# Optimization experiments

Hardware: AMD Instinct MI355X
Metric: run time of the kernel (lower is better)

## Reference

```python
import jax, jax.numpy as jnp
import numpy as np

N = 400000          # num nodes == num edges (required by the module's final cat)
E = 400000
NODE_DIM = 64
BOND_DIM = 16
HIDDEN = 128
DEPTH = 5


def _sanitize(t):
    return jnp.nan_to_num(t, nan=0.0, posinf=1000.0, neginf=-1000.0)


def setup_inputs() -> dict:
    key = jax.random.key(0)
    ks = jax.random.split(key, 10)
    x = jax.random.normal(ks[0], (N, NODE_DIM), dtype=jnp.float32)
    edge_attr = jax.random.normal(ks[1], (E, BOND_DIM), dtype=jnp.float32)
    edge_index = jax.random.randint(ks[2], (2, E), 0, N, dtype=jnp.int32)
    # edges come in reverse pairs (2k, 2k+1): force endpoints consistent
    src = edge_index[0]
    dst = edge_index[1]
    # make edge 2k+1 the reverse of edge 2k
    src = src.reshape(E // 2, 2)
    dst = dst.reshape(E // 2, 2)
    src = jnp.stack([src[:, 0], dst[:, 0]], axis=1).reshape(E)
    dst = jnp.stack([dst[:, 0], src.reshape(E // 2, 2)[:, 0]], axis=1).reshape(E)
    edge_index = jnp.stack([src, dst], axis=0)
    rev_edge_index = jnp.arange(E, dtype=jnp.int32) ^ 1
    # parameters (kaiming-normal-ish scale, zero bias as in reset_parameters)
    def kaiming(k, fan_in, fan_out):
        std = np.sqrt(2.0 / fan_out)  # mode='fan_out'
        return std * jax.random.normal(k, (fan_in, fan_out), dtype=jnp.float32)
    W_i = kaiming(ks[3], NODE_DIM + BOND_DIM, HIDDEN)
    b_i = jnp.zeros((HIDDEN,), dtype=jnp.float32)
    W_h = kaiming(ks[4], HIDDEN, HIDDEN)
    b_h = jnp.zeros((HIDDEN,), dtype=jnp.float32)
    W_o = kaiming(ks[5], NODE_DIM + HIDDEN, HIDDEN)
    b_o = jnp.zeros((HIDDEN,), dtype=jnp.float32)
    return {"x": x, "edge_index": edge_index, "edge_attr": edge_attr,
            "rev_edge_index": rev_edge_index,
            "W_i": W_i, "b_i": b_i, "W_h": W_h, "b_h": b_h,
            "W_o": W_o, "b_o": b_o}


def reference(x, edge_index, edge_attr, rev_edge_index, W_i, b_i, W_h, b_h, W_o, b_o):
    src, dst = edge_index[0], edge_index[1]
    # h0: per-edge hidden state [E, H]
    h0 = jax.nn.relu(jnp.concatenate([x[src], edge_attr], axis=1) @ W_i + b_i)
    h = h0
    for _ in range(1, DEPTH):
        # scatter-add incoming messages at dst node ids (rows >= N stay 0)
        m = jnp.zeros_like(h).at[dst].add(h)
        # subtract reverse-edge message at src node ids (all rev indices valid)
        m = m.at[src].add(-h[rev_edge_index])
        m = _sanitize(m) @ W_h + b_h
        h = jax.nn.relu(h0 + m)   # dropout is identity in eval / p handled as 0
    m_final = jnp.zeros_like(h).at[dst].add(h)
    h_cat = jnp.concatenate([x, _sanitize(m_final)], axis=1)  # requires N == E
    out = jax.nn.relu(h_cat @ W_o + b_o)
    return _sanitize(out)
```

## Files before the change

### kernel.cpp

```cpp
#include <hip/hip_runtime.h>


typedef __bf16 bf16x8 __attribute__((ext_vector_type(8)));
typedef float f32x4 __attribute__((ext_vector_type(4)));
typedef unsigned short u16;
typedef unsigned int u32;

#define LDW  104
#define LDW2 200
#define LDT  136
#define SLOTS 16

static __device__ __forceinline__ u16 f32_to_bf16(float f) {
    union { float f; u32 u; } c; c.f = f;
    u32 u = c.u;
    u += 0x7FFFu + ((u >> 16) & 1u);
    return (u16)(u >> 16);
}
static __device__ __forceinline__ u32 pk2(float a, float b) {
    return (u32)f32_to_bf16(a) | (((u32)f32_to_bf16(b)) << 16);
}
static __device__ __forceinline__ uint4 pack8(float4 a, float4 b) {
    return make_uint4(pk2(a.x, a.y), pk2(a.z, a.w), pk2(b.x, b.y), pk2(b.z, b.w));
}


__global__ __launch_bounds__(256) void k_prep(
    const float4* __restrict__ x4, const float4* __restrict__ ea4,
    const float* __restrict__ Wi, const float* __restrict__ Wo,
    uint4* __restrict__ cnt16, uint4* __restrict__ xb4,
    uint4* __restrict__ eab4, u16* __restrict__ WiT, u16* __restrict__ WoT,
    int nCnt16, int nX8, int nEa8)
{
    const int gtid = blockIdx.x * 256 + threadIdx.x;
    const int stride = gridDim.x * 256;
    const uint4 z = make_uint4(0, 0, 0, 0);
    for (int i = gtid; i < nCnt16; i += stride) cnt16[i] = z;
    for (int i = gtid; i < nX8; i += stride)
        xb4[i] = pack8(x4[2 * i], x4[2 * i + 1]);
    for (int i = gtid; i < nEa8; i += stride)
        eab4[i] = pack8(ea4[2 * i], ea4[2 * i + 1]);
    for (int i = gtid; i < 128 * LDW; i += stride) {
        int n = i / LDW, k = i - n * LDW;
        WiT[i] = (k < 80) ? f32_to_bf16(Wi[k * 128 + n]) : (u16)0;
    }
    for (int i = gtid; i < 128 * LDW2; i += stride) {
        int n = i / LDW2, k = i - n * LDW2;
        WoT[i] = (k < 192) ? f32_to_bf16(Wo[k * 128 + n]) : (u16)0;
    }
}

__global__ __launch_bounds__(256) void k_fill(
    const int* __restrict__ ei, int* __restrict__ counts,
    int2* __restrict__ slot, int E)
{
    const int e = blockIdx.x * 256 + threadIdx.x;
    if (e < E) {
        const int dst = ei[E + e];
        const int pos = atomicAdd(&counts[dst], 1);
        if (pos < SLOTS)
            slot[(size_t)dst * SLOTS + pos] = make_int2(ei[e], e);
    }
}

__global__ __launch_bounds__(512) void k_main(
    const u16* __restrict__ xb, const u16* __restrict__ eab,
    const int2* __restrict__ slot, const int* __restrict__ deg,
    const uint4* __restrict__ WiT16, const uint4* __restrict__ WoT16,
    const float* __restrict__ bi, const float* __restrict__ bh,
    const float* __restrict__ bo, float* __restrict__ out, int Nn)
{
    __shared__ __align__(16) u16 sWi[128 * LDW];
    __shared__ __align__(16) u16 sWo[128 * LDW2];
    __shared__ __align__(16) u16 sTr[8][16 * LDT];

    const int tid  = threadIdx.x;
    const int wave = tid >> 6;
    const int lane = tid & 63;
    const int col  = lane & 15;
    const int quad = lane >> 4;

    #pragma unroll 2
    for (int i = tid; i < 128 * LDW / 8; i += 512)
        ((uint4*)sWi)[i] = WiT16[i];
    #pragma unroll 2
    for (int i = tid; i < 128 * LDW2 / 8; i += 512)
        ((uint4*)sWo)[i] = WoT16[i];
    __syncthreads();

    float bias_i[8], bias_h[8], bias_o[8];
    #pragma unroll
    for (int nt = 0; nt < 8; ++nt) {
        bias_i[nt] = bi[nt * 16 + col];
        bias_h[nt] = bh[nt * 16 + col];
        bias_o[nt] = bo[nt * 16 + col];
    }

    u16* tr = &sTr[wave][0];
    const uint4 z4 = make_uint4(0, 0, 0, 0);

    for (int t4 = 0; t4 < 4; ++t4) {
        const int row0 = blockIdx.x * 512 + wave * 64 + t4 * 16;
        const int nA   = row0 + col;
        int degA = (nA < Nn) ? min(deg[nA], SLOTS) : 0;
        int degC[4];
        #pragma unroll
        for (int rg = 0; rg < 4; ++rg) {
            int n = row0 + quad * 4 + rg;
            degC[rg] = (n < Nn) ? min(deg[n], SLOTS) : 0;
        }
        int tmax = degA;
        tmax = max(tmax, __shfl_xor(tmax, 1));
        tmax = max(tmax, __shfl_xor(tmax, 2));
        tmax = max(tmax, __shfl_xor(tmax, 4));
        tmax = max(tmax, __shfl_xor(tmax, 8));

        f32x4 m[8];
        #pragma unroll
        for (int nt = 0; nt < 8; ++nt) m[nt] = (f32x4)0.0f;

        for (int t = 0; t < tmax; ++t) {
            uint4 Af0 = z4, Af1 = z4, Af2 = z4;
            if (t < degA) {
                const int2 se = slot[(size_t)nA * SLOTS + t];
                const u16* xr = xb + (size_t)se.x * 64;
                Af0 = *(const uint4*)(xr + quad * 8);
                Af1 = *(const uint4*)(xr + 32 + quad * 8);
                if (quad < 2)
                    Af2 = *(const uint4*)(eab + (size_t)se.y * 16 + quad * 8);
            }
            f32x4 acc[8];
            #pragma unroll
            for (int nt = 0; nt < 8; ++nt) acc[nt] = (f32x4)0.0f;
            const uint4 Af[3] = {Af0, Af1, Af2};
            #pragma unroll
            for (int ks = 0; ks < 3; ++ks) {
                bf16x8 a = __builtin_bit_cast(bf16x8, Af[ks]);
                #pragma unroll
                for (int nt = 0; nt < 8; ++nt) {
                    bf16x8 b = __builtin_bit_cast(bf16x8,
                        *(const uint4*)(&sWi[(nt * 16 + col) * LDW + ks * 32 + quad * 8]));
                    acc[nt] = __builtin_amdgcn_mfma_f32_16x16x32_bf16(a, b, acc[nt], 0, 0, 0);
                }
            }
            #pragma unroll
            for (int nt = 0; nt < 8; ++nt) {
                #pragma unroll
                for (int rg = 0; rg < 4; ++rg) {
                    float h = fmaxf(fmaxf(acc[nt][rg] + bias_i[nt], 0.0f)
                                    + bias_h[nt], 0.0f);
                    m[nt][rg] += (t < degC[rg]) ? h : 0.0f;
                }
            }
        }

        asm volatile("s_waitcnt lgkmcnt(0)" ::: "memory");
        #pragma unroll
        for (int nt = 0; nt < 8; ++nt) {
            #pragma unroll
            for (int rg = 0; rg < 4; ++rg)
                tr[(quad * 4 + rg) * LDT + nt * 16 + col] = f32_to_bf16(m[nt][rg]);
        }
        asm volatile("s_waitcnt lgkmcnt(0)" ::: "memory");
        __builtin_amdgcn_sched_barrier(0);

        const u16* xrs = xb + (size_t)min(nA, Nn - 1) * 64;
        uint4 Bf[6];
        Bf[0] = *(const uint4*)(xrs + quad * 8);
        Bf[1] = *(const uint4*)(xrs + 32 + quad * 8);
        #pragma unroll
        for (int ks = 2; ks < 6; ++ks)
            Bf[ks] = *(const uint4*)(&tr[col * LDT + (ks - 2) * 32 + quad * 8]);

        f32x4 acc2[8];
        #pragma unroll
        for (int nt = 0; nt < 8; ++nt) acc2[nt] = (f32x4)0.0f;
        #pragma unroll
        for (int ks = 0; ks < 6; ++ks) {
            bf16x8 a = __builtin_bit_cast(bf16x8, Bf[ks]);
            #pragma unroll
            for (int nt = 0; nt < 8; ++nt) {
                bf16x8 b = __builtin_bit_cast(bf16x8,
                    *(const uint4*)(&sWo[(nt * 16 + col) * LDW2 + ks * 32 + quad * 8]));
                acc2[nt] = __builtin_amdgcn_mfma_f32_16x16x32_bf16(a, b, acc2[nt], 0, 0, 0);
            }
        }

        #pragma unroll
        for (int rg = 0; rg < 4; ++rg) {
            int node = row0 + quad * 4 + rg;
            if (node < Nn) {
                float* orow = out + (size_t)node * 128;
                #pragma unroll
                for (int nt = 0; nt < 8; ++nt) {
                    float o = fmaxf(acc2[nt][rg] + bias_o[nt], 0.0f);
                    float op = __shfl_xor(o, 1);
                    if ((col & 1) == 0)
                        *(float2*)(orow + nt * 16 + col) = make_float2(o, op);
                }
            }
        }
    }
}


__global__ __launch_bounds__(256) void k_zero_fb(uint4* __restrict__ out, int n16)
{
    const uint4 z = make_uint4(0, 0, 0, 0);
    for (int i = blockIdx.x * blockDim.x + threadIdx.x; i < n16;
         i += gridDim.x * blockDim.x)
        out[i] = z;
}

__global__ __launch_bounds__(256) void k_edge_fb(
    const float* __restrict__ x, const float* __restrict__ ea,
    const int* __restrict__ ei, const float* __restrict__ Wi,
    const float* __restrict__ bi, const float* __restrict__ bh,
    float* __restrict__ macc, int E)
{
    __shared__ __align__(16) u16 sW[128 * LDW];
    const int tid  = threadIdx.x;
    const int wave = tid >> 6;
    const int lane = tid & 63;
    const int col  = lane & 15;
    const int quad = lane >> 4;

    for (int i = tid; i < 96 * 128; i += 256) {
        int k = i >> 7, n = i & 127;
        sW[n * LDW + k] = (k < 80) ? f32_to_bf16(Wi[i]) : (u16)0;
    }
    __syncthreads();

    float bias_i[8], bias_h[8];
    #pragma unroll
    for (int nt = 0; nt < 8; ++nt) {
        bias_i[nt] = bi[nt * 16 + col];
        bias_h[nt] = bh[nt * 16 + col];
    }

    for (int t = 0; t < 4; ++t) {
        const int e0 = blockIdx.x * 256 + wave * 64 + t * 16;
        const int eidx = e0 + col;
        const int ec = (eidx < E) ? eidx : (E - 1);
        const int src = ei[ec];
        const float* xr = x + (size_t)src * 64;
        uint4 A0 = pack8(*(const float4*)(xr + quad * 8),
                         *(const float4*)(xr + quad * 8 + 4));
        uint4 A1 = pack8(*(const float4*)(xr + 32 + quad * 8),
                         *(const float4*)(xr + 32 + quad * 8 + 4));
        uint4 A2 = make_uint4(0, 0, 0, 0);
        if (quad < 2) {
            const float* er = ea + (size_t)ec * 16 + quad * 8;
            A2 = pack8(*(const float4*)er, *(const float4*)(er + 4));
        }

        f32x4 acc[8];
        #pragma unroll
        for (int nt = 0; nt < 8; ++nt) acc[nt] = (f32x4)0.0f;
        const uint4 Af[3] = {A0, A1, A2};
        #pragma unroll
        for (int ks = 0; ks < 3; ++ks) {
            bf16x8 a = __builtin_bit_cast(bf16x8, Af[ks]);
            #pragma unroll
            for (int nt = 0; nt < 8; ++nt) {
                bf16x8 b = __builtin_bit_cast(bf16x8,
                    *(const uint4*)(&sW[(nt * 16 + col) * LDW + ks * 32 + quad * 8]));
                acc[nt] = __builtin_amdgcn_mfma_f32_16x16x32_bf16(a, b, acc[nt], 0, 0, 0);
            }
        }
        #pragma unroll
        for (int rg = 0; rg < 4; ++rg) {
            int e = e0 + quad * 4 + rg;
            if (e < E) {
                int dst = ei[E + e];
                float* mrow = macc + (size_t)dst * 128;
                #pragma unroll
                for (int nt = 0; nt < 8; ++nt) {
                    float h = fmaxf(fmaxf(acc[nt][rg] + bias_i[nt], 0.0f)
                                    + bias_h[nt], 0.0f);
                    atomicAdd(mrow + nt * 16 + col, h);
                }
            }
        }
    }
}

__global__ __launch_bounds__(256) void k_node_fb(
    const float* __restrict__ x, const float* __restrict__ Wo,
    const float* __restrict__ bo, float* __restrict__ outv, int Nn)
{
    __shared__ __align__(16) u16 sW[128 * LDW2];
    const int tid  = threadIdx.x;
    const int wave = tid >> 6;
    const int lane = tid & 63;
    const int col  = lane & 15;
    const int quad = lane >> 4;

    for (int i = tid; i < 192 * 128; i += 256) {
        int k = i >> 7, n = i & 127;
        sW[n * LDW2 + k] = f32_to_bf16(Wo[i]);
    }
    __syncthreads();

    float bias[8];
    #pragma unroll
    for (int nt = 0; nt < 8; ++nt) bias[nt] = bo[nt * 16 + col];

    for (int t = 0; t < 4; ++t) {
        const int row0 = blockIdx.x * 256 + wave * 64 + t * 16;
        const int nodea = row0 + col;
        const int na = (nodea < Nn) ? nodea : (Nn - 1);
        const float* xr = x + (size_t)na * 64;
        uint4 Af[6];
        Af[0] = pack8(*(const float4*)(xr + quad * 8),
                      *(const float4*)(xr + quad * 8 + 4));
        Af[1] = pack8(*(const float4*)(xr + 32 + quad * 8),
                      *(const float4*)(xr + 32 + quad * 8 + 4));
        const float* mr = outv + (size_t)na * 128;
        #pragma unroll
        for (int ks = 2; ks < 6; ++ks) {
            const float* p = mr + (ks - 2) * 32 + quad * 8;
            Af[ks] = pack8(*(const float4*)p, *(const float4*)(p + 4));
        }

        f32x4 acc[8];
        #pragma unroll
        for (int nt = 0; nt < 8; ++nt) acc[nt] = (f32x4)0.0f;
        #pragma unroll
        for (int ks = 0; ks < 6; ++ks) {
            bf16x8 a = __builtin_bit_cast(bf16x8, Af[ks]);
            #pragma unroll
            for (int nt = 0; nt < 8; ++nt) {
                bf16x8 b = __builtin_bit_cast(bf16x8,
                    *(const uint4*)(&sW[(nt * 16 + col) * LDW2 + ks * 32 + quad * 8]));
                acc[nt] = __builtin_amdgcn_mfma_f32_16x16x32_bf16(a, b, acc[nt], 0, 0, 0);
            }
        }
        #pragma unroll
        for (int rg = 0; rg < 4; ++rg) {
            int node = row0 + quad * 4 + rg;
            if (node < Nn) {
                float* orow = outv + (size_t)node * 128;
                #pragma unroll
                for (int nt = 0; nt < 8; ++nt)
                    orow[nt * 16 + col] = fmaxf(acc[nt][rg] + bias[nt], 0.0f);
            }
        }
    }
}


extern "C" void kernel_launch(void* const* d_in, const int* in_sizes, int n_in,
                              void* d_out, int out_size, void* d_ws, size_t ws_size,
                              hipStream_t stream)
{
    const float* x  = (const float*)d_in[0];
    const int*   ei = (const int*)d_in[1];
    const float* ea = (const float*)d_in[2];
    const float* Wi = (const float*)d_in[4];
    const float* bi = (const float*)d_in[5];
    const float* bh = (const float*)d_in[7];
    const float* Wo = (const float*)d_in[8];
    const float* bo = (const float*)d_in[9];
    float* outp = (float*)d_out;

    const int N = in_sizes[0] / 64;
    const int E = in_sizes[1] / 2;

    const size_t off_slot = (size_t)N * 4;
    const size_t off_xb   = off_slot + (size_t)N * SLOTS * 8;
    const size_t off_eab  = off_xb   + (size_t)N * 64 * 2;
    const size_t off_wit  = off_eab  + (size_t)E * 16 * 2;
    const size_t off_wot  = off_wit  + (size_t)128 * LDW * 2;
    const size_t need     = off_wot  + (size_t)128 * LDW2 * 2;

    const int blocksE = (E + 255) / 256;
    const int blocksM = (N + 511) / 512;

    if (ws_size >= need) {
        char* ws = (char*)d_ws;
        int*  counts = (int*)ws;
        int2* slot   = (int2*)(ws + off_slot);
        u16*  xb     = (u16*)(ws + off_xb);
        u16*  eab    = (u16*)(ws + off_eab);
        u16*  WiT    = (u16*)(ws + off_wit);
        u16*  WoT    = (u16*)(ws + off_wot);

        hipLaunchKernelGGL(k_prep, dim3(4096), dim3(256), 0, stream,
                           (const float4*)x, (const float4*)ea, Wi, Wo,
                           (uint4*)counts, (uint4*)xb, (uint4*)eab, WiT, WoT,
                           N / 4, N * 8, E * 2);
        hipLaunchKernelGGL(k_fill, dim3(blocksE), dim3(256), 0, stream,
                           ei, counts, slot, E);
        hipLaunchKernelGGL(k_main, dim3(blocksM), dim3(512), 0, stream,
                           xb, eab, slot, counts,
                           (const uint4*)WiT, (const uint4*)WoT,
                           bi, bh, bo, outp, N);
    } else {
        const int blocks2 = (N + 255) / 256;
        hipLaunchKernelGGL(k_zero_fb, dim3(1024), dim3(256), 0, stream,
                           (uint4*)outp, N * 32);
        hipLaunchKernelGGL(k_edge_fb, dim3(blocksE), dim3(256), 0, stream,
                           x, ea, ei, Wi, bi, bh, outp, E);
        hipLaunchKernelGGL(k_node_fb, dim3(blocks2), dim3(256), 0, stream,
                           x, Wo, bo, outp, N);
    }
}
```

Measured before the change: 508.2 us.

## Split fused gather-GEMM kernel into separate edge and node kernels

The single fused kernel, which aggregated incoming edge messages and then ran the output GEMM from a per-wave LDS transpose, is split in two. The first kernel computes per-node message sums and writes them to a bf16 workspace buffer. The second kernel reads x and that buffer and runs the output GEMM with nontemporal stores. This cuts LDS use per block (no sWo or transpose tile alongside sWi), which should raise occupancy, at the cost of an extra global round trip of N×128 bf16 values and one more launch.

```diff
diff --git a/kernel.cpp b/kernel.cpp
--- a/kernel.cpp
+++ b/kernel.cpp
@@ -3,12 +3,12 @@
 
 typedef __bf16 bf16x8 __attribute__((ext_vector_type(8)));
 typedef float f32x4 __attribute__((ext_vector_type(4)));
+typedef float f32x2 __attribute__((ext_vector_type(2)));
 typedef unsigned short u16;
 typedef unsigned int u32;
 
 #define LDW  104
 #define LDW2 200
-#define LDT  136
 #define SLOTS 16
 
 static __device__ __forceinline__ u16 f32_to_bf16(float f) {
@@ -63,16 +63,14 @@
     }
 }
 
-__global__ __launch_bounds__(512) void k_main(
+__global__ __launch_bounds__(256) void k_edge_r(
     const u16* __restrict__ xb, const u16* __restrict__ eab,
     const int2* __restrict__ slot, const int* __restrict__ deg,
-    const uint4* __restrict__ WiT16, const uint4* __restrict__ WoT16,
+    const uint4* __restrict__ WiT16,
     const float* __restrict__ bi, const float* __restrict__ bh,
-    const float* __restrict__ bo, float* __restrict__ out, int Nn)
+    u16* __restrict__ mout, int Nn)
 {
     __shared__ __align__(16) u16 sWi[128 * LDW];
-    __shared__ __align__(16) u16 sWo[128 * LDW2];
-    __shared__ __align__(16) u16 sTr[8][16 * LDT];
 
     const int tid  = threadIdx.x;
     const int wave = tid >> 6;
@@ -80,27 +78,22 @@
     const int col  = lane & 15;
     const int quad = lane >> 4;
 
-    #pragma unroll 2
-    for (int i = tid; i < 128 * LDW / 8; i += 512)
+    #pragma unroll 4
+    for (int i = tid; i < 128 * LDW / 8; i += 256)
         ((uint4*)sWi)[i] = WiT16[i];
-    #pragma unroll 2
-    for (int i = tid; i < 128 * LDW2 / 8; i += 512)
-        ((uint4*)sWo)[i] = WoT16[i];
     __syncthreads();
 
-    float bias_i[8], bias_h[8], bias_o[8];
+    float bias_i[8], bias_h[8];
     #pragma unroll
     for (int nt = 0; nt < 8; ++nt) {
         bias_i[nt] = bi[nt * 16 + col];
         bias_h[nt] = bh[nt * 16 + col];
-        bias_o[nt] = bo[nt * 16 + col];
-    }
-
-    u16* tr = &sTr[wave][0];
+    }
+
     const uint4 z4 = make_uint4(0, 0, 0, 0);
 
     for (int t4 = 0; t4 < 4; ++t4) {
-        const int row0 = blockIdx.x * 512 + wave * 64 + t4 * 16;
+        const int row0 = blockIdx.x * 256 + wave * 64 + t4 * 16;
         const int nA   = row0 + col;
         int degA = (nA < Nn) ? min(deg[nA], SLOTS) : 0;
         int degC[4];
@@ -154,35 +147,68 @@
             }
         }
 
-        asm volatile("s_waitcnt lgkmcnt(0)" ::: "memory");
-        #pragma unroll
-        for (int nt = 0; nt < 8; ++nt) {
-            #pragma unroll
-            for (int rg = 0; rg < 4; ++rg)
-                tr[(quad * 4 + rg) * LDT + nt * 16 + col] = f32_to_bf16(m[nt][rg]);
-        }
-        asm volatile("s_waitcnt lgkmcnt(0)" ::: "memory");
-        __builtin_amdgcn_sched_barrier(0);
-
-        const u16* xrs = xb + (size_t)min(nA, Nn - 1) * 64;
-        uint4 Bf[6];
-        Bf[0] = *(const uint4*)(xrs + quad * 8);
-        Bf[1] = *(const uint4*)(xrs + 32 + quad * 8);
+        #pragma unroll
+        for (int rg = 0; rg < 4; ++rg) {
+            int node = row0 + quad * 4 + rg;
+            u16* mrow = mout + (size_t)node * 128;
+            #pragma unroll
+            for (int nt = 0; nt < 8; ++nt) {
+                float v  = m[nt][rg];
+                float vp = __shfl_xor(v, 1);
+                if (node < Nn && (col & 1) == 0)
+                    *(u32*)(mrow + nt * 16 + col) = pk2(v, vp);
+            }
+        }
+    }
+}
+
+__global__ __launch_bounds__(256) void k_node_f2(
+    const u16* __restrict__ xb, const u16* __restrict__ mb,
+    const uint4* __restrict__ WoT16, const float* __restrict__ bo,
+    float* __restrict__ out, int Nn)
+{
+    __shared__ __align__(16) u16 sWo[128 * LDW2];
+    const int tid  = threadIdx.x;
+    const int wave = tid >> 6;
+    const int lane = tid & 63;
+    const int col  = lane & 15;
+    const int quad = lane >> 4;
+
+    #pragma unroll 4
+    for (int i = tid; i < 128 * LDW2 / 8; i += 256)
+        ((uint4*)sWo)[i] = WoT16[i];
+    __syncthreads();
+
+    float bias[8];
+    #pragma unroll
+    for (int nt = 0; nt < 8; ++nt) bias[nt] = bo[nt * 16 + col];
+
+    for (int t = 0; t < 4; ++t) {
+        const int row0 = blockIdx.x * 256 + wave * 64 + t * 16;
+        const int nodea = row0 + col;
+        const int na = (nodea < Nn) ? nodea : (Nn - 1);
+
+        const u16* xr = xb + (size_t)na * 64;
+        uint4 Af[6];
+        Af[0] = *(const uint4*)(xr + quad * 8);
+        Af[1] = *(const uint4*)(xr + 32 + quad * 8);
+        const u16* mr = mb + (size_t)na * 128;
         #pragma unroll
         for (int ks = 2; ks < 6; ++ks)
-            Bf[ks] = *(const uint4*)(&tr[col * LDT + (ks - 2) * 32 + quad * 8]);
-
-        f32x4 acc2[8];
-        #pragma unroll
-        for (int nt = 0; nt < 8; ++nt) acc2[nt] = (f32x4)0.0f;
+            Af[ks] = *(const uint4*)(mr + (ks - 2) * 32 + quad * 8);
+
+        f32x4 acc[8];
+        #pragma unroll
+        for (int nt = 0; nt < 8; ++nt) acc[nt] = (f32x4)0.0f;
+
         #pragma unroll
         for (int ks = 0; ks < 6; ++ks) {
-            bf16x8 a = __builtin_bit_cast(bf16x8, Bf[ks]);
+            bf16x8 a = __builtin_bit_cast(bf16x8, Af[ks]);
             #pragma unroll
             for (int nt = 0; nt < 8; ++nt) {
                 bf16x8 b = __builtin_bit_cast(bf16x8,
                     *(const uint4*)(&sWo[(nt * 16 + col) * LDW2 + ks * 32 + quad * 8]));
-                acc2[nt] = __builtin_amdgcn_mfma_f32_16x16x32_bf16(a, b, acc2[nt], 0, 0, 0);
+                acc[nt] = __builtin_amdgcn_mfma_f32_16x16x32_bf16(a, b, acc[nt], 0, 0, 0);
             }
         }
 
@@ -193,10 +219,13 @@
                 float* orow = out + (size_t)node * 128;
                 #pragma unroll
                 for (int nt = 0; nt < 8; ++nt) {
-                    float o = fmaxf(acc2[nt][rg] + bias_o[nt], 0.0f);
+                    float o = fmaxf(acc[nt][rg] + bias[nt], 0.0f);
                     float op = __shfl_xor(o, 1);
-                    if ((col & 1) == 0)
-                        *(float2*)(orow + nt * 16 + col) = make_float2(o, op);
+                    if ((col & 1) == 0) {
+                        f32x2 v2; v2.x = o; v2.y = op;
+                        __builtin_nontemporal_store(v2,
+                            (f32x2*)(orow + nt * 16 + col));
+                    }
                 }
             }
         }
@@ -370,12 +399,13 @@
     const size_t off_slot = (size_t)N * 4;
     const size_t off_xb   = off_slot + (size_t)N * SLOTS * 8;
     const size_t off_eab  = off_xb   + (size_t)N * 64 * 2;
-    const size_t off_wit  = off_eab  + (size_t)E * 16 * 2;
+    const size_t off_m    = off_eab  + (size_t)E * 16 * 2;
+    const size_t off_wit  = off_m    + (size_t)N * 128 * 2;
     const size_t off_wot  = off_wit  + (size_t)128 * LDW * 2;
     const size_t need     = off_wot  + (size_t)128 * LDW2 * 2;
 
     const int blocksE = (E + 255) / 256;
-    const int blocksM = (N + 511) / 512;
+    const int blocksN = (N + 255) / 256;
 
     if (ws_size >= need) {
         char* ws = (char*)d_ws;
@@ -383,6 +413,7 @@
         int2* slot   = (int2*)(ws + off_slot);
         u16*  xb     = (u16*)(ws + off_xb);
         u16*  eab    = (u16*)(ws + off_eab);
+        u16*  mbuf   = (u16*)(ws + off_m);
         u16*  WiT    = (u16*)(ws + off_wit);
         u16*  WoT    = (u16*)(ws + off_wot);
 
@@ -392,17 +423,17 @@
                            N / 4, N * 8, E * 2);
         hipLaunchKernelGGL(k_fill, dim3(blocksE), dim3(256), 0, stream,
                            ei, counts, slot, E);
-        hipLaunchKernelGGL(k_main, dim3(blocksM), dim3(512), 0, stream,
-                           xb, eab, slot, counts,
-                           (const uint4*)WiT, (const uint4*)WoT,
-                           bi, bh, bo, outp, N);
+        hipLaunchKernelGGL(k_edge_r, dim3(blocksN), dim3(256), 0, stream,
+                           xb, eab, slot, counts, (const uint4*)WiT,
+                           bi, bh, mbuf, N);
+        hipLaunchKernelGGL(k_node_f2, dim3(blocksN), dim3(256), 0, stream,
+                           xb, mbuf, (const uint4*)WoT, bo, outp, N);
     } else {
-        const int blocks2 = (N + 255) / 256;
         hipLaunchKernelGGL(k_zero_fb, dim3(1024), dim3(256), 0, stream,
                            (uint4*)outp, N * 32);
         hipLaunchKernelGGL(k_edge_fb, dim3(blocksE), dim3(256), 0, stream,
                            x, ea, ei, Wi, bi, bh, outp, E);
-        hipLaunchKernelGGL(k_node_fb, dim3(blocks2), dim3(256), 0, stream,
+        hipLaunchKernelGGL(k_node_fb, dim3(blocksN), dim3(256), 0, stream,
                            x, Wo, bo, outp, N);
     }
 }
```

Measured after the change: 553.1 us. 1.09x slower.
